# Kernel tuning notes

Hardware: AMD Instinct MI355X
Metric: run time of the kernel (lower is better)

The kernel has to match this reference:

```python
import jax, jax.numpy as jnp
import numpy as np


def hard_sigmoid(x):
    # clamp(0.2*x + 0.5, 0, 1) -- Theano/lwtnn convention
    return jnp.clip(0.2 * x + 0.5, 0.0, 1.0)


def setup_inputs() -> dict:
    key = jax.random.key(0)
    ks = jax.random.split(key, 10)
    B, T, D, H = 128, 1024, 256, 256
    s_in = 1.0 / np.sqrt(D)
    s_h = 1.0 / np.sqrt(H)
    return {
        "x": jax.random.normal(ks[0], (B, T, D), dtype=jnp.float32),
        "W_z": jax.random.normal(ks[1], (D, H), dtype=jnp.float32) * s_in,
        "W_r": jax.random.normal(ks[2], (D, H), dtype=jnp.float32) * s_in,
        "W_h": jax.random.normal(ks[3], (D, H), dtype=jnp.float32) * s_in,
        "U_z": jax.random.normal(ks[4], (H, H), dtype=jnp.float32) * s_h,
        "U_r": jax.random.normal(ks[5], (H, H), dtype=jnp.float32) * s_h,
        "U_h": jax.random.normal(ks[6], (H, H), dtype=jnp.float32) * s_h,
        "b_z": jax.random.normal(ks[7], (H,), dtype=jnp.float32) * 0.01,
        "b_r": jax.random.normal(ks[8], (H,), dtype=jnp.float32) * 0.01,
        "b_h": jax.random.normal(ks[9], (H,), dtype=jnp.float32) * 0.01,
    }


def reference(x, W_z, W_r, W_h, U_z, U_r, U_h, b_z, b_r, b_h):
    B, T, D = x.shape
    H = W_z.shape[1]
    # Precompute input projections for all timesteps in one big GEMM each
    # (same math as per-step xt @ W_* in the original loop).
    xz = jnp.einsum("btd,dh->bth", x, W_z) + b_z  # [B,T,H]
    xr = jnp.einsum("btd,dh->bth", x, W_r) + b_r
    xh = jnp.einsum("btd,dh->bth", x, W_h) + b_h

    def step(h, inputs):
        xz_t, xr_t, xh_t = inputs  # each [B,H]
        z = hard_sigmoid(xz_t + h @ U_z)
        r = hard_sigmoid(xr_t + h @ U_r)
        hh = jnp.tanh(xh_t + (r * h) @ U_h)
        h_new = z * h + (1.0 - z) * hh
        return h_new, None

    h0 = jnp.zeros((B, H), dtype=x.dtype)
    # scan over time axis: move T to leading axis
    xs = (xz.swapaxes(0, 1), xr.swapaxes(0, 1), xh.swapaxes(0, 1))
    h_final, _ = jax.lax.scan(step, h0, xs)
    return h_final
```

## Files before the change

### kernel.cpp

```cpp
#include <hip/hip_runtime.h>
#include <hip/hip_bf16.h>
#include <math.h>

#define BB 128
#define TT 1024
#define DD 256
#define HH 256
#define MM (BB * TT)
#define NN3 768

typedef __attribute__((ext_vector_type(8))) short short8;
typedef __attribute__((ext_vector_type(4))) float f32x4;
typedef __attribute__((address_space(1))) unsigned int gu32;
typedef __attribute__((address_space(3))) unsigned int lu32;

static __device__ __forceinline__ float bf2f(unsigned int u16) {
    return __uint_as_float(u16 << 16);
}
static __device__ __forceinline__ unsigned short f2bf(float f) {
    unsigned int u = __float_as_uint(f);
    unsigned int r = u + 0x7FFFu + ((u >> 16) & 1u);
    return (unsigned short)(r >> 16);
}
static __device__ __forceinline__ unsigned short f2bf_fast(float f) {
    return (unsigned short)((__float_as_uint(f) + 0x8000u) >> 16);
}

static __device__ __forceinline__ void barrier_lgkm() {
    asm volatile("s_waitcnt lgkmcnt(0)\n\ts_barrier" ::: "memory");
}
static __device__ __forceinline__ void barrier_full() {
    asm volatile("s_waitcnt vmcnt(0) lgkmcnt(0)\n\ts_barrier" ::: "memory");
}

__global__ __launch_bounds__(256) void wb_kernel(
    const float* __restrict__ Wz, const float* __restrict__ Wr,
    const float* __restrict__ Wh, unsigned short* __restrict__ Wb)
{
    int n = blockIdx.x;
    int g = n >> 8, col = n & 255;
    const float* W = (g == 0) ? Wz : (g == 1 ? Wr : Wh);
    int k = threadIdx.x;
    Wb[(size_t)n * 256 + k] = f2bf(W[(size_t)k * HH + col]);
}

__global__ __launch_bounds__(256)
__attribute__((amdgpu_waves_per_eu(2, 2)))
void xproj_mfma(
    const float* __restrict__ x, const unsigned short* __restrict__ Wb,
    const float* __restrict__ bz, const float* __restrict__ br,
    const float* __restrict__ bh, unsigned short* __restrict__ xw)
{
    const int tid  = threadIdx.x;
    const int lane = tid & 63;
    const int wv   = tid >> 6;
    const int nq   = lane & 15;
    const int kq   = lane >> 4;

    const int n0  = blockIdx.x * 64;
    const int m0  = blockIdx.y * 128;
    const int g   = n0 >> 8;
    const int nc0 = n0 & 255;
    const float* bias = (g == 0) ? bz : (g == 1 ? br : bh);

    short8 wf[8][4];
#pragma unroll
    for (int c = 0; c < 8; ++c)
#pragma unroll
        for (int nt = 0; nt < 4; ++nt)
            wf[c][nt] = *(const short8*)&Wb[(size_t)(n0 + nt * 16 + nq) * 256
                                            + c * 32 + kq * 8];
    float bv[4];
#pragma unroll
    for (int nt = 0; nt < 4; ++nt) bv[nt] = bias[nc0 + nt * 16 + nq];

    f32x4 acc[2][4];
#pragma unroll
    for (int mi = 0; mi < 2; ++mi)
#pragma unroll
        for (int nt = 0; nt < 4; ++nt) acc[mi][nt] = (f32x4){0.f, 0.f, 0.f, 0.f};

    const int mrow0 = m0 + wv * 32;

#pragma unroll
    for (int c = 0; c < 8; ++c) {
        short8 af[2];
#pragma unroll
        for (int mi = 0; mi < 2; ++mi) {
            const float* xp = &x[(size_t)(mrow0 + mi * 16 + nq) * 256
                                 + c * 32 + kq * 8];
            float4 f0 = *(const float4*)xp;
            float4 f1 = *(const float4*)(xp + 4);
            short8 a;
            a[0] = (short)f2bf(f0.x); a[1] = (short)f2bf(f0.y);
            a[2] = (short)f2bf(f0.z); a[3] = (short)f2bf(f0.w);
            a[4] = (short)f2bf(f1.x); a[5] = (short)f2bf(f1.y);
            a[6] = (short)f2bf(f1.z); a[7] = (short)f2bf(f1.w);
            af[mi] = a;
        }
#pragma unroll
        for (int mi = 0; mi < 2; ++mi)
#pragma unroll
            for (int nt = 0; nt < 4; ++nt)
                acc[mi][nt] = __builtin_amdgcn_mfma_f32_16x16x32_bf16(
                    af[mi], wf[c][nt], acc[mi][nt], 0, 0, 0);
    }

    const int t0   = (m0 & 1023) + wv * 32;
    const int b    = m0 >> 10;
    const int bid  = b >> 4;
    const int brow = b & 15;
    const int lane4 = (brow >> 2) * 16 + nq;
    const int ii    = brow & 3;

#pragma unroll
    for (int mi = 0; mi < 2; ++mi)
#pragma unroll
        for (int nt = 0; nt < 4; ++nt) {
            int ti = g * 16 + (nc0 >> 4) + nt;
#pragma unroll
            for (int i = 0; i < 4; ++i) {
                int t = t0 + mi * 16 + kq * 4 + i;
                size_t addr = (size_t)(t * 8 + bid) * 12288
                              + (size_t)(ti * 256 + lane4 * 4 + ii);
                xw[addr] = f2bf(acc[mi][nt][i] + bv[nt]);
            }
        }
}

__global__ __launch_bounds__(1024)
__attribute__((amdgpu_waves_per_eu(4, 4)))
void gru_rec_kernel(
    const unsigned short* __restrict__ xw,
    const float* __restrict__ Uz, const float* __restrict__ Ur,
    const float* __restrict__ Uh,
    float* __restrict__ out)
{
    __shared__ unsigned short xstage[2][12288];
    __shared__ short hA[16][264];
    __shared__ short rhA[16][264];

    const int tid  = threadIdx.x;
    const int lane = tid & 63;
    const int wv   = tid >> 6;
    const int nq   = lane & 15;
    const int kq   = lane >> 4;
    const int bid  = blockIdx.x;
    const int col0 = wv * 16;

    short8 wz[8], wr[8], whv[8];
#pragma unroll
    for (int c = 0; c < 8; ++c) {
        short8 fz, fr, fh;
#pragma unroll
        for (int j = 0; j < 8; ++j) {
            size_t rowoff = (size_t)(c * 32 + kq * 8 + j) * HH + col0 + nq;
            fz[j] = (short)f2bf(Uz[rowoff]);
            fr[j] = (short)f2bf(Ur[rowoff]);
            fh[j] = (short)f2bf(Uh[rowoff]);
        }
        wz[c] = fz; wr[c] = fr; whv[c] = fh;
    }

    for (int idx = tid; idx < 16 * 264; idx += 1024) ((short*)hA)[idx] = 0;
    float hprev[4];
#pragma unroll
    for (int i = 0; i < 4; ++i) hprev[i] = 0.f;

    auto stage = [&](int t, int buf) {
        if (wv < 12) {
            const char* gsrc = (const char*)(xw + (size_t)(t * 8 + bid) * 12288);
            char* lbase = (char*)&xstage[buf][0];
            int woff = wv * 2048;
#pragma unroll
            for (int ld = 0; ld < 2; ++ld) {
                int off = woff + ld * 1024;
                __builtin_amdgcn_global_load_lds(
                    (const gu32*)(gsrc + off + lane * 16),
                    (lu32*)(lbase + off), 16, 0, 0);
            }
        }
    };

    stage(0, 0);
    barrier_full();

    auto step = [&](int t, int par) {
        int tn2 = (t + 1 < TT) ? (t + 1) : (TT - 1);
        stage(tn2, par ^ 1);

        const unsigned short* xs = &xstage[par][0];

        f32x4 accZ, accR;
        {
            uint2 uz = *(const uint2*)&xs[((0  + wv) * 64 + lane) * 4];
            uint2 ur = *(const uint2*)&xs[((16 + wv) * 64 + lane) * 4];
            accZ[0] = bf2f(uz.x & 0xffffu);
            accZ[1] = bf2f(uz.x >> 16);
            accZ[2] = bf2f(uz.y & 0xffffu);
            accZ[3] = bf2f(uz.y >> 16);
            accR[0] = bf2f(ur.x & 0xffffu);
            accR[1] = bf2f(ur.x >> 16);
            accR[2] = bf2f(ur.y & 0xffffu);
            accR[3] = bf2f(ur.y >> 16);
        }
#pragma unroll
        for (int c = 0; c < 8; ++c) {
            short8 af = *(const short8*)&hA[nq][c * 32 + kq * 8];
            accZ = __builtin_amdgcn_mfma_f32_16x16x32_bf16(af, wz[c], accZ, 0, 0, 0);
            accR = __builtin_amdgcn_mfma_f32_16x16x32_bf16(af, wr[c], accR, 0, 0, 0);
        }

#pragma unroll
        for (int i = 0; i < 4; ++i) {
            float r = __builtin_amdgcn_fmed3f(
                __builtin_fmaf(0.2f, accR[i], 0.5f), 0.f, 1.f);
            rhA[kq * 4 + i][col0 + nq] = (short)f2bf_fast(r * hprev[i]);
        }
        barrier_lgkm();

        f32x4 accH;
        {
            uint2 u = *(const uint2*)&xs[((32 + wv) * 64 + lane) * 4];
            accH[0] = bf2f(u.x & 0xffffu);
            accH[1] = bf2f(u.x >> 16);
            accH[2] = bf2f(u.y & 0xffffu);
            accH[3] = bf2f(u.y >> 16);
        }
#pragma unroll
        for (int c = 0; c < 8; ++c) {
            short8 af = *(const short8*)&rhA[nq][c * 32 + kq * 8];
            accH = __builtin_amdgcn_mfma_f32_16x16x32_bf16(af, whv[c], accH, 0, 0, 0);
        }

#pragma unroll
        for (int i = 0; i < 4; ++i) {
            float z = __builtin_amdgcn_fmed3f(
                __builtin_fmaf(0.2f, accZ[i], 0.5f), 0.f, 1.f);
            float a = __builtin_amdgcn_fmed3f(accH[i], -12.f, 12.f);
            float e  = exp2f(a * 2.88539008f);
            float hh = __builtin_fmaf(-2.f, __builtin_amdgcn_rcpf(e + 1.f), 1.f);
            float hn = __builtin_fmaf(z, hprev[i] - hh, hh);
            hprev[i] = hn;
            hA[kq * 4 + i][col0 + nq] = (short)f2bf_fast(hn);
        }
        barrier_full();
    };

    for (int t = 0; t < TT; t += 2) {
        step(t, 0);
        step(t + 1, 1);
    }

#pragma unroll
    for (int i = 0; i < 4; ++i)
        out[(size_t)(bid * 16 + kq * 4 + i) * HH + col0 + nq] = hprev[i];
}

extern "C" void kernel_launch(void* const* d_in, const int* in_sizes, int n_in,
                              void* d_out, int out_size, void* d_ws, size_t ws_size,
                              hipStream_t stream) {
    const float* x  = (const float*)d_in[0];
    const float* Wz = (const float*)d_in[1];
    const float* Wr = (const float*)d_in[2];
    const float* Wh = (const float*)d_in[3];
    const float* Uz = (const float*)d_in[4];
    const float* Ur = (const float*)d_in[5];
    const float* Uh = (const float*)d_in[6];
    const float* bz = (const float*)d_in[7];
    const float* br = (const float*)d_in[8];
    const float* bh = (const float*)d_in[9];
    float* out = (float*)d_out;

    unsigned short* xw = (unsigned short*)d_ws;
    unsigned short* Wb =
        (unsigned short*)((char*)d_ws + (size_t)MM * NN3 * sizeof(unsigned short));

    wb_kernel<<<NN3, 256, 0, stream>>>(Wz, Wr, Wh, Wb);

    dim3 g1(NN3 / 64, MM / 128);
    xproj_mfma<<<g1, 256, 0, stream>>>(x, Wb, bz, br, bh, xw);

    gru_rec_kernel<<<8, 1024, 0, stream>>>(xw, Uz, Ur, Uh, out);
}
```

Measured before the change: 2.828 ms.

## Restructure input projection to reuse x tiles and write packed outputs; split tanh accumulator chain

The input-projection kernel now loads and converts each x tile to bf16 once. It then loops over all 48 output column tiles, streaming weights from global memory, instead of reloading x for every 64-column block. Output stores become packed 8-byte writes that match the recurrent kernel's staging layout, replacing scattered 2-byte stores. In the recurrent kernel, the dependent MFMA chain for the candidate gate is split into two interleaved accumulators to cut serial latency. The trade-off is more weight traffic per block and fewer blocks (1024) in the projection.

```diff
diff --git a/kernel.cpp b/kernel.cpp
--- a/kernel.cpp
+++ b/kernel.cpp
@@ -57,38 +57,17 @@
     const int nq   = lane & 15;
     const int kq   = lane >> 4;
 
-    const int n0  = blockIdx.x * 64;
-    const int m0  = blockIdx.y * 128;
-    const int g   = n0 >> 8;
-    const int nc0 = n0 & 255;
-    const float* bias = (g == 0) ? bz : (g == 1 ? br : bh);
-
-    short8 wf[8][4];
-#pragma unroll
-    for (int c = 0; c < 8; ++c)
-#pragma unroll
-        for (int nt = 0; nt < 4; ++nt)
-            wf[c][nt] = *(const short8*)&Wb[(size_t)(n0 + nt * 16 + nq) * 256
-                                            + c * 32 + kq * 8];
-    float bv[4];
-#pragma unroll
-    for (int nt = 0; nt < 4; ++nt) bv[nt] = bias[nc0 + nt * 16 + nq];
-
-    f32x4 acc[2][4];
-#pragma unroll
-    for (int mi = 0; mi < 2; ++mi)
-#pragma unroll
-        for (int nt = 0; nt < 4; ++nt) acc[mi][nt] = (f32x4){0.f, 0.f, 0.f, 0.f};
-
-    const int mrow0 = m0 + wv * 32;
-
-#pragma unroll
-    for (int c = 0; c < 8; ++c) {
-        short8 af[2];
-#pragma unroll
-        for (int mi = 0; mi < 2; ++mi) {
-            const float* xp = &x[(size_t)(mrow0 + mi * 16 + nq) * 256
-                                 + c * 32 + kq * 8];
+    const int bid = blockIdx.x >> 7;
+    const int t0  = (blockIdx.x & 127) * 8;
+    const int tw0 = t0 + wv * 2;
+
+    short8 af[8][2];
+#pragma unroll
+    for (int mi = 0; mi < 2; ++mi) {
+        const float* xrow = &x[((size_t)(bid * 16 + nq) * 1024 + (tw0 + mi)) * 256];
+#pragma unroll
+        for (int c = 0; c < 8; ++c) {
+            const float* xp = xrow + c * 32 + kq * 8;
             float4 f0 = *(const float4*)xp;
             float4 f1 = *(const float4*)(xp + 4);
             short8 a;
@@ -96,36 +75,44 @@
             a[2] = (short)f2bf(f0.z); a[3] = (short)f2bf(f0.w);
             a[4] = (short)f2bf(f1.x); a[5] = (short)f2bf(f1.y);
             a[6] = (short)f2bf(f1.z); a[7] = (short)f2bf(f1.w);
-            af[mi] = a;
-        }
-#pragma unroll
-        for (int mi = 0; mi < 2; ++mi)
-#pragma unroll
-            for (int nt = 0; nt < 4; ++nt)
-                acc[mi][nt] = __builtin_amdgcn_mfma_f32_16x16x32_bf16(
-                    af[mi], wf[c][nt], acc[mi][nt], 0, 0, 0);
-    }
-
-    const int t0   = (m0 & 1023) + wv * 32;
-    const int b    = m0 >> 10;
-    const int bid  = b >> 4;
-    const int brow = b & 15;
-    const int lane4 = (brow >> 2) * 16 + nq;
-    const int ii    = brow & 3;
-
-#pragma unroll
-    for (int mi = 0; mi < 2; ++mi)
-#pragma unroll
-        for (int nt = 0; nt < 4; ++nt) {
-            int ti = g * 16 + (nc0 >> 4) + nt;
-#pragma unroll
-            for (int i = 0; i < 4; ++i) {
-                int t = t0 + mi * 16 + kq * 4 + i;
-                size_t addr = (size_t)(t * 8 + bid) * 12288
-                              + (size_t)(ti * 256 + lane4 * 4 + ii);
-                xw[addr] = f2bf(acc[mi][nt][i] + bv[nt]);
+            af[c][mi] = a;
+        }
+    }
+
+#pragma unroll
+    for (int g = 0; g < 3; ++g) {
+        const float* bias = (g == 0) ? bz : (g == 1 ? br : bh);
+#pragma unroll 2
+        for (int s = 0; s < 16; ++s) {
+            const int st = g * 16 + s;
+            short8 wf[8];
+#pragma unroll
+            for (int c = 0; c < 8; ++c)
+                wf[c] = *(const short8*)&Wb[(size_t)(st * 16 + nq) * 256
+                                            + c * 32 + kq * 8];
+            const float bv = bias[s * 16 + nq];
+
+            f32x4 acc0 = (f32x4){0.f, 0.f, 0.f, 0.f};
+            f32x4 acc1 = (f32x4){0.f, 0.f, 0.f, 0.f};
+#pragma unroll
+            for (int c = 0; c < 8; ++c) {
+                acc0 = __builtin_amdgcn_mfma_f32_16x16x32_bf16(af[c][0], wf[c], acc0, 0, 0, 0);
+                acc1 = __builtin_amdgcn_mfma_f32_16x16x32_bf16(af[c][1], wf[c], acc1, 0, 0, 0);
             }
-        }
+
+#pragma unroll
+            for (int mi = 0; mi < 2; ++mi) {
+                f32x4 a = (mi == 0) ? acc0 : acc1;
+                unsigned int lo = (unsigned int)f2bf(a[0] + bv)
+                                | ((unsigned int)f2bf(a[1] + bv) << 16);
+                unsigned int hi = (unsigned int)f2bf(a[2] + bv)
+                                | ((unsigned int)f2bf(a[3] + bv) << 16);
+                uint2 val; val.x = lo; val.y = hi;
+                *(uint2*)&xw[(size_t)((tw0 + mi) * 8 + bid) * 12288
+                             + st * 256 + kq * 64 + nq * 4] = val;
+            }
+        }
+    }
 }
 
 __global__ __launch_bounds__(1024)
@@ -219,25 +206,29 @@
         }
         barrier_lgkm();
 
-        f32x4 accH;
+        f32x4 accH0, accH1;
         {
             uint2 u = *(const uint2*)&xs[((32 + wv) * 64 + lane) * 4];
-            accH[0] = bf2f(u.x & 0xffffu);
-            accH[1] = bf2f(u.x >> 16);
-            accH[2] = bf2f(u.y & 0xffffu);
-            accH[3] = bf2f(u.y >> 16);
+            accH0[0] = bf2f(u.x & 0xffffu);
+            accH0[1] = bf2f(u.x >> 16);
+            accH0[2] = bf2f(u.y & 0xffffu);
+            accH0[3] = bf2f(u.y >> 16);
+            accH1 = (f32x4){0.f, 0.f, 0.f, 0.f};
         }
 #pragma unroll
         for (int c = 0; c < 8; ++c) {
             short8 af = *(const short8*)&rhA[nq][c * 32 + kq * 8];
-            accH = __builtin_amdgcn_mfma_f32_16x16x32_bf16(af, whv[c], accH, 0, 0, 0);
+            if (c & 1)
+                accH1 = __builtin_amdgcn_mfma_f32_16x16x32_bf16(af, whv[c], accH1, 0, 0, 0);
+            else
+                accH0 = __builtin_amdgcn_mfma_f32_16x16x32_bf16(af, whv[c], accH0, 0, 0, 0);
         }
 
 #pragma unroll
         for (int i = 0; i < 4; ++i) {
             float z = __builtin_amdgcn_fmed3f(
                 __builtin_fmaf(0.2f, accZ[i], 0.5f), 0.f, 1.f);
-            float a = __builtin_amdgcn_fmed3f(accH[i], -12.f, 12.f);
+            float a = __builtin_amdgcn_fmed3f(accH0[i] + accH1[i], -12.f, 12.f);
             float e  = exp2f(a * 2.88539008f);
             float hh = __builtin_fmaf(-2.f, __builtin_amdgcn_rcpf(e + 1.f), 1.f);
             float hn = __builtin_fmaf(z, hprev[i] - hh, hh);
@@ -278,8 +269,7 @@
 
     wb_kernel<<<NN3, 256, 0, stream>>>(Wz, Wr, Wh, Wb);
 
-    dim3 g1(NN3 / 64, MM / 128);
-    xproj_mfma<<<g1, 256, 0, stream>>>(x, Wb, bz, br, bh, xw);
+    xproj_mfma<<<1024, 256, 0, stream>>>(x, Wb, bz, br, bh, xw);
 
     gru_rec_kernel<<<8, 1024, 0, stream>>>(xw, Uz, Ur, Uh, out);
 }
```

Result: slower. 3.148 ms (+11.3%).
